# Optimization experiments

Hardware: AMD Instinct MI355X
Metric: run time of the kernel (lower is better)

Reference implementation:

```python
import math
import jax, jax.numpy as jnp
import numpy as np

K, B, T = 6, 8, 12
DIM = 256
DH = 64          # dim_head
NH = 8           # num_heads
G = 8            # offset_groups
INNER = DH * NH  # 512
HALF = INNER // 2  # 256
OFF_D = INNER // G  # 64
HBEV = WBEV = 256
PW = PH = 102.4   # x/y range extents
SCALE = DH ** -0.5
OFF_SCALE = 4.0


def setup_inputs() -> dict:
    key = jax.random.key(0)
    ks = jax.random.split(key, 20)
    w = lambda i, shape: jax.random.normal(ks[i], shape, jnp.float32) * 0.05
    return {
        "dec_embed": jax.random.normal(ks[0], (K, B, T, DIM), jnp.float32),
        "bev_feat": jax.random.normal(ks[1], (B, DIM, HBEV, WBEV), jnp.float32),
        "query_scale": jax.random.uniform(ks[2], (K, B, T, HALF), jnp.float32),
        "ref_points": (jax.random.uniform(ks[3], (K, B, T, 2), jnp.float32) * 2.0 - 1.0) * 51.2,
        "Wq": w(4, (DIM, HALF)), "bq": jnp.zeros((HALF,), jnp.float32),
        "Wk": w(5, (DIM, HALF)),
        "Wv": w(6, (DIM, HALF)),
        "pq_W1": w(7, (HALF, HALF)), "pq_b1": jnp.zeros((HALF,), jnp.float32),
        "pq_W2": w(8, (HALF, HALF)), "pq_b2": jnp.zeros((HALF,), jnp.float32),
        "pk_W1": w(9, (HALF, HALF)), "pk_b1": jnp.zeros((HALF,), jnp.float32),
        "pk_W2": w(10, (HALF, HALF)), "pk_b2": jnp.zeros((HALF,), jnp.float32),
        "off_W1": w(11, (OFF_D // 2, OFF_D)), "off_b1": jnp.zeros((OFF_D,), jnp.float32),
        "off_W2": w(12, (OFF_D, 2)), "off_b2": jnp.zeros((2,), jnp.float32),
        "out_W": w(13, (HALF, DIM)), "out_b": jnp.zeros((DIM,), jnp.float32),
    }


def _grid_sample(im, grid):
    """F.grid_sample, bilinear, padding_mode='zeros', align_corners=False.
    im: (B,C,H,W), grid: (B,Hg,Wg,2) with (x,y) in [-1,1]. Returns (B,C,Hg,Wg)."""
    Bn, C, Hh, Ww = im.shape
    gx, gy = grid[..., 0], grid[..., 1]
    ix = ((gx + 1.0) * Ww - 1.0) * 0.5
    iy = ((gy + 1.0) * Hh - 1.0) * 0.5
    ix0 = jnp.floor(ix)
    iy0 = jnp.floor(iy)
    wx = (ix - ix0)[:, None]  # (B,1,Hg,Wg)
    wy = (iy - iy0)[:, None]
    imf = im.reshape(Bn, C, Hh * Ww)

    def gather(xq, yq):
        valid = (xq >= 0) & (xq < Ww) & (yq >= 0) & (yq < Hh)
        idx = (jnp.clip(yq, 0, Hh - 1) * Ww + jnp.clip(xq, 0, Ww - 1)).astype(jnp.int32)
        v = jnp.take_along_axis(imf, idx.reshape(Bn, 1, -1), axis=2)
        v = v.reshape(Bn, C, *xq.shape[1:])
        return v * valid[:, None].astype(im.dtype)

    v00 = gather(ix0, iy0)
    v01 = gather(ix0 + 1, iy0)
    v10 = gather(ix0, iy0 + 1)
    v11 = gather(ix0 + 1, iy0 + 1)
    return (v00 * (1 - wx) * (1 - wy) + v01 * wx * (1 - wy)
            + v10 * (1 - wx) * wy + v11 * wx * wy)


def _sine_embed(pos, hidden=256, temp=40.0):
    """DAB-DETR style sine embedding for 2D positions. pos: (...,2) -> (...,hidden)."""
    half = hidden // 2
    dim_t = jnp.arange(half, dtype=pos.dtype)
    dim_t = temp ** (2.0 * jnp.floor(dim_t / 2.0) / half)
    sc = 2.0 * math.pi
    ex = pos[..., 0, None] * sc / dim_t
    ey = pos[..., 1, None] * sc / dim_t

    def interleave(e):
        return jnp.stack((jnp.sin(e[..., 0::2]), jnp.cos(e[..., 1::2])), axis=-1).reshape(*e.shape[:-1], -1)

    return jnp.concatenate((interleave(ey), interleave(ex)), axis=-1)


def reference(dec_embed, bev_feat, query_scale, ref_points,
              Wq, bq, Wk, Wv,
              pq_W1, pq_b1, pq_W2, pq_b2,
              pk_W1, pk_b1, pk_W2, pk_b2,
              off_W1, off_b1, off_W2, off_b2,
              out_W, out_b):
    de = dec_embed.transpose(1, 0, 2, 3)     # (B,K,T,D)
    qs = query_scale.transpose(1, 0, 2, 3)   # (B,K,T,256)
    rp = ref_points.transpose(1, 0, 2, 3)    # (B,K,T,2)
    Bn, Kn, Tn = de.shape[:3]

    con_q = de @ Wq + bq                                    # (B,K,T,256)
    oin = con_q.reshape(Bn, Kn, Tn, G, OFF_D // 2)          # (B,K,T,G,32)
    off = jax.nn.gelu(oin @ off_W1 + off_b1, approximate=False)
    off = jnp.tanh(off @ off_W2 + off_b2) * OFF_SCALE       # (B,K,T,G,2)

    vgrid = rp[..., None, :] + off                          # (B,K,T,G,2)
    vgrid = vgrid.reshape(Bn, Kn * Tn, G, 2)
    norm = jnp.array([2.0 / PW, 2.0 / PH], vgrid.dtype)
    vgrid_scaled = vgrid * norm                             # ref_from_Q normalization

    con_k_map = jnp.einsum('bchw,cd->bdhw', bev_feat, Wk)   # 1x1 conv, no bias
    v_map = jnp.einsum('bchw,cd->bdhw', bev_feat, Wv)
    con_k = _grid_sample(con_k_map, vgrid_scaled)           # (B,256,KT,G)
    v = _grid_sample(v_map, vgrid_scaled)                   # (B,256,KT,G)

    ref_scaled = rp * norm                                  # (B,K,T,2)
    qse = _sine_embed(ref_scaled)                           # (B,K,T,256)
    pos_q = (jax.nn.relu(qse @ pq_W1 + pq_b1) @ pq_W2 + pq_b2) * qs
    kse = _sine_embed(vgrid_scaled)                         # (B,KT,G,256)
    pos_k = jax.nn.relu(kse @ pk_W1 + pk_b1) @ pk_W2 + pk_b2

    BS = Bn * Kn * Tn
    dh = HALF // NH  # 32 per-head content dim
    cq = con_q.reshape(BS, 1, NH, dh)
    pq = pos_q.reshape(BS, 1, NH, dh)
    ck = con_k.transpose(0, 2, 3, 1).reshape(BS, G, NH, dh)
    pk = pos_k.reshape(BS, G, NH, dh)
    vv = v.transpose(0, 2, 3, 1).reshape(BS, G, NH, dh)

    q = jnp.concatenate([cq, pq], -1).transpose(0, 2, 1, 3) * SCALE  # (BS,NH,1,64)
    k = jnp.concatenate([ck, pk], -1).transpose(0, 2, 1, 3)          # (BS,NH,G,64)
    vv = vv.transpose(0, 2, 1, 3)                                    # (BS,NH,G,32)

    sim = jnp.einsum('bhid,bhjd->bhij', q, k)               # (BS,NH,1,G)
    attn = jax.nn.softmax(sim, axis=-1)
    out = jnp.einsum('bhij,bhjd->bhid', attn, vv)           # (BS,NH,1,32)

    out = out.transpose(0, 2, 1, 3).reshape(Bn, Kn, Tn, HALF).transpose(1, 0, 2, 3)
    out = out @ out_W + out_b                               # (K,B,T,D)
    return dec_embed + out
```

## Files before the change

kernel.cpp:

```cpp
#include <hip/hip_runtime.h>
#include <math.h>

#define NK 6
#define NB 8
#define NT 12
#define D 256
#define NG 8
#define NHD 8
#define HW 256
#define NQ (NK*NB*NT)

__global__ __launch_bounds__(256)
void dca_kernel(const float* __restrict__ dec_embed,
                const float* __restrict__ bev_feat,
                const float* __restrict__ query_scale,
                const float* __restrict__ ref_points,
                const float* __restrict__ Wq,     const float* __restrict__ bq,
                const float* __restrict__ Wk,     const float* __restrict__ Wv,
                const float* __restrict__ pq_W1,  const float* __restrict__ pq_b1,
                const float* __restrict__ pq_W2,  const float* __restrict__ pq_b2,
                const float* __restrict__ pk_W1,  const float* __restrict__ pk_b1,
                const float* __restrict__ pk_W2,  const float* __restrict__ pk_b2,
                const float* __restrict__ off_W1, const float* __restrict__ off_b1,
                const float* __restrict__ off_W2, const float* __restrict__ off_b2,
                const float* __restrict__ out_W,  const float* __restrict__ out_b,
                float* __restrict__ out)
{
    __shared__ float de[D];
    __shared__ float conq[D];
    __shared__ float qse[D];
    __shared__ float tmp1[D];
    __shared__ float posq[D];
    __shared__ float oatt[D];
    __shared__ float h1[NG][64];
    __shared__ float gxy[NG][2];
    __shared__ float sim[NHD][NG];
    __shared__ float bufA[NG][D];
    __shared__ float bufB[NG][D];
    __shared__ float conk[NG][D];
    __shared__ float vmat[NG][D];

    const int tid = threadIdx.x;
    const int q   = blockIdx.x;
    const int bb  = (q / NT) % NB;

    const float NORM = 0.01953125f;
    const float TWO_PI = 6.28318530717958647692f;
    const float L2_40_OVER_64 = 5.32192809488736234787f / 64.0f;

    de[tid] = dec_embed[(size_t)q * D + tid];
    __syncthreads();

    {
        float acc = bq[tid];
        #pragma unroll 4
        for (int i = 0; i < D; i += 4) {
            float4 d4 = *(const float4*)&de[i];
            acc += d4.x * Wq[(i + 0) * D + tid];
            acc += d4.y * Wq[(i + 1) * D + tid];
            acc += d4.z * Wq[(i + 2) * D + tid];
            acc += d4.w * Wq[(i + 3) * D + tid];
        }
        conq[tid] = acc;
    }
    __syncthreads();

    for (int idx = tid; idx < NG * 64; idx += 256) {
        int g = idx >> 6, j = idx & 63;
        float acc = off_b1[j];
        #pragma unroll
        for (int i = 0; i < 32; i += 4) {
            float4 c4 = *(const float4*)&conq[g * 32 + i];
            acc += c4.x * off_W1[(i + 0) * 64 + j];
            acc += c4.y * off_W1[(i + 1) * 64 + j];
            acc += c4.z * off_W1[(i + 2) * 64 + j];
            acc += c4.w * off_W1[(i + 3) * 64 + j];
        }
        h1[g][j] = 0.5f * acc * (1.0f + erff(acc * 0.70710678118654752440f));
    }
    __syncthreads();

    if (tid < NG * 2) {
        int g = tid >> 1, c = tid & 1;
        float acc = off_b2[c];
        #pragma unroll
        for (int j = 0; j < 64; j += 4) {
            float4 hh = *(const float4*)&h1[g][j];
            acc += hh.x * off_W2[(j + 0) * 2 + c];
            acc += hh.y * off_W2[(j + 1) * 2 + c];
            acc += hh.z * off_W2[(j + 2) * 2 + c];
            acc += hh.w * off_W2[(j + 3) * 2 + c];
        }
        float off = tanhf(acc) * 4.0f;
        float rp  = ref_points[(size_t)q * 2 + c];
        gxy[g][c] = (rp + off) * NORM;
    }
    __syncthreads();

    {
        const float* ch = bev_feat + ((size_t)bb * D + tid) * HW * HW;
        #pragma unroll
        for (int g = 0; g < NG; ++g) {
            float gx = gxy[g][0], gy = gxy[g][1];
            float ix = ((gx + 1.0f) * HW - 1.0f) * 0.5f;
            float iy = ((gy + 1.0f) * HW - 1.0f) * 0.5f;
            float fx0 = floorf(ix), fy0 = floorf(iy);
            float wx = ix - fx0, wy = iy - fy0;
            int x0 = (int)fx0, y0 = (int)fy0;
            bool xin0 = (x0 >= 0) && (x0 < HW);
            bool xin1 = (x0 + 1 >= 0) && (x0 + 1 < HW);
            bool yin0 = (y0 >= 0) && (y0 < HW);
            bool yin1 = (y0 + 1 >= 0) && (y0 + 1 < HW);
            float v00 = 0.f, v01 = 0.f, v10 = 0.f, v11 = 0.f;
            if (yin0) {
                if (xin0) v00 = ch[y0 * HW + x0];
                if (xin1) v01 = ch[y0 * HW + x0 + 1];
            }
            if (yin1) {
                if (xin0) v10 = ch[(y0 + 1) * HW + x0];
                if (xin1) v11 = ch[(y0 + 1) * HW + x0 + 1];
            }
            bufA[g][tid] = v00 * (1.f - wx) * (1.f - wy) + v01 * wx * (1.f - wy)
                         + v10 * (1.f - wx) * wy        + v11 * wx * wy;
        }
        {
            float rx = ref_points[(size_t)q * 2 + 0] * NORM;
            float ry = ref_points[(size_t)q * 2 + 1] * NORM;
            int j = tid;
            float pos = (j < 128) ? ry : rx;
            int m = (j & 127) >> 1;
            float freq = TWO_PI / exp2f((float)m * L2_40_OVER_64);
            float e = pos * freq;
            qse[j] = (j & 1) ? cosf(e) : sinf(e);
        }
        {
            int m = (tid & 127) >> 1;
            float freq = TWO_PI / exp2f((float)m * L2_40_OVER_64);
            #pragma unroll
            for (int g = 0; g < NG; ++g) {
                float pos = (tid < 128) ? gxy[g][1] : gxy[g][0];
                float e = pos * freq;
                bufB[g][tid] = (tid & 1) ? cosf(e) : sinf(e);
            }
        }
    }
    __syncthreads();

    {
        float accK[NG], accV[NG];
        #pragma unroll
        for (int g = 0; g < NG; ++g) { accK[g] = 0.f; accV[g] = 0.f; }
        #pragma unroll 2
        for (int i = 0; i < D; i += 4) {
            float wk0 = Wk[(i + 0) * D + tid], wk1 = Wk[(i + 1) * D + tid];
            float wk2 = Wk[(i + 2) * D + tid], wk3 = Wk[(i + 3) * D + tid];
            float wv0 = Wv[(i + 0) * D + tid], wv1 = Wv[(i + 1) * D + tid];
            float wv2 = Wv[(i + 2) * D + tid], wv3 = Wv[(i + 3) * D + tid];
            #pragma unroll
            for (int g = 0; g < NG; ++g) {
                float4 s = *(const float4*)&bufA[g][i];
                accK[g] += s.x * wk0 + s.y * wk1 + s.z * wk2 + s.w * wk3;
                accV[g] += s.x * wv0 + s.y * wv1 + s.z * wv2 + s.w * wv3;
            }
        }
        #pragma unroll
        for (int g = 0; g < NG; ++g) { conk[g][tid] = accK[g]; vmat[g][tid] = accV[g]; }
    }
    __syncthreads();

    {
        float acc[NG + 1];
        float biask = pk_b1[tid];
        #pragma unroll
        for (int g = 0; g < NG; ++g) acc[g] = biask;
        acc[NG] = pq_b1[tid];
        #pragma unroll 2
        for (int i = 0; i < D; i += 4) {
            float k0 = pk_W1[(i + 0) * D + tid], k1 = pk_W1[(i + 1) * D + tid];
            float k2 = pk_W1[(i + 2) * D + tid], k3 = pk_W1[(i + 3) * D + tid];
            float q0 = pq_W1[(i + 0) * D + tid], q1 = pq_W1[(i + 1) * D + tid];
            float q2 = pq_W1[(i + 2) * D + tid], q3 = pq_W1[(i + 3) * D + tid];
            #pragma unroll
            for (int g = 0; g < NG; ++g) {
                float4 s = *(const float4*)&bufB[g][i];
                acc[g] += s.x * k0 + s.y * k1 + s.z * k2 + s.w * k3;
            }
            float4 t = *(const float4*)&qse[i];
            acc[NG] += t.x * q0 + t.y * q1 + t.z * q2 + t.w * q3;
        }
        #pragma unroll
        for (int g = 0; g < NG; ++g) bufA[g][tid] = fmaxf(acc[g], 0.f);
        tmp1[tid] = fmaxf(acc[NG], 0.f);
    }
    __syncthreads();

    {
        float acc[NG + 1];
        float biask = pk_b2[tid];
        #pragma unroll
        for (int g = 0; g < NG; ++g) acc[g] = biask;
        acc[NG] = pq_b2[tid];
        #pragma unroll 2
        for (int i = 0; i < D; i += 4) {
            float k0 = pk_W2[(i + 0) * D + tid], k1 = pk_W2[(i + 1) * D + tid];
            float k2 = pk_W2[(i + 2) * D + tid], k3 = pk_W2[(i + 3) * D + tid];
            float q0 = pq_W2[(i + 0) * D + tid], q1 = pq_W2[(i + 1) * D + tid];
            float q2 = pq_W2[(i + 2) * D + tid], q3 = pq_W2[(i + 3) * D + tid];
            #pragma unroll
            for (int g = 0; g < NG; ++g) {
                float4 s = *(const float4*)&bufA[g][i];
                acc[g] += s.x * k0 + s.y * k1 + s.z * k2 + s.w * k3;
            }
            float4 t = *(const float4*)&tmp1[i];
            acc[NG] += t.x * q0 + t.y * q1 + t.z * q2 + t.w * q3;
        }
        #pragma unroll
        for (int g = 0; g < NG; ++g) bufB[g][tid] = acc[g];
        posq[tid] = acc[NG] * query_scale[(size_t)q * D + tid];
    }
    __syncthreads();

    if (tid < NHD * NG) {
        int h = tid >> 3, g = tid & 7;
        float s = 0.f;
        #pragma unroll
        for (int d = 0; d < 32; d += 4) {
            float4 a = *(const float4*)&conq[h * 32 + d];
            float4 b = *(const float4*)&conk[g][h * 32 + d];
            float4 c = *(const float4*)&posq[h * 32 + d];
            float4 e = *(const float4*)&bufB[g][h * 32 + d];
            s += a.x * b.x + a.y * b.y + a.z * b.z + a.w * b.w;
            s += c.x * e.x + c.y * e.y + c.z * e.z + c.w * e.w;
        }
        sim[h][g] = s * 0.125f;
    }
    __syncthreads();

    if (tid < NHD) {
        int h = tid;
        float mx = sim[h][0];
        for (int g = 1; g < NG; ++g) mx = fmaxf(mx, sim[h][g]);
        float ex[NG], sum = 0.f;
        #pragma unroll
        for (int g = 0; g < NG; ++g) { ex[g] = expf(sim[h][g] - mx); sum += ex[g]; }
        float inv = 1.0f / sum;
        #pragma unroll
        for (int g = 0; g < NG; ++g) sim[h][g] = ex[g] * inv;
    }
    __syncthreads();

    {
        int h = tid >> 5, d = tid & 31;
        float o = 0.f;
        #pragma unroll
        for (int g = 0; g < NG; ++g) o += sim[h][g] * vmat[g][h * 32 + d];
        oatt[tid] = o;
    }
    __syncthreads();

    {
        float acc = out_b[tid];
        #pragma unroll 4
        for (int i = 0; i < D; i += 4) {
            float4 o4 = *(const float4*)&oatt[i];
            acc += o4.x * out_W[(i + 0) * D + tid];
            acc += o4.y * out_W[(i + 1) * D + tid];
            acc += o4.z * out_W[(i + 2) * D + tid];
            acc += o4.w * out_W[(i + 3) * D + tid];
        }
        out[(size_t)q * D + tid] = acc + de[tid];
    }
}

extern "C" void kernel_launch(void* const* d_in, const int* in_sizes, int n_in,
                              void* d_out, int out_size, void* d_ws, size_t ws_size,
                              hipStream_t stream) {
    const float* dec_embed   = (const float*)d_in[0];
    const float* bev_feat    = (const float*)d_in[1];
    const float* query_scale = (const float*)d_in[2];
    const float* ref_points  = (const float*)d_in[3];
    const float* Wq     = (const float*)d_in[4];
    const float* bq     = (const float*)d_in[5];
    const float* Wk     = (const float*)d_in[6];
    const float* Wv     = (const float*)d_in[7];
    const float* pq_W1  = (const float*)d_in[8];
    const float* pq_b1  = (const float*)d_in[9];
    const float* pq_W2  = (const float*)d_in[10];
    const float* pq_b2  = (const float*)d_in[11];
    const float* pk_W1  = (const float*)d_in[12];
    const float* pk_b1  = (const float*)d_in[13];
    const float* pk_W2  = (const float*)d_in[14];
    const float* pk_b2  = (const float*)d_in[15];
    const float* off_W1 = (const float*)d_in[16];
    const float* off_b1 = (const float*)d_in[17];
    const float* off_W2 = (const float*)d_in[18];
    const float* off_b2 = (const float*)d_in[19];
    const float* out_W  = (const float*)d_in[20];
    const float* out_b  = (const float*)d_in[21];
    float* out = (float*)d_out;

    dca_kernel<<<NQ, 256, 0, stream>>>(dec_embed, bev_feat, query_scale, ref_points,
                                       Wq, bq, Wk, Wv,
                                       pq_W1, pq_b1, pq_W2, pq_b2,
                                       pk_W1, pk_b1, pk_W2, pk_b2,
                                       off_W1, off_b1, off_W2, off_b2,
                                       out_W, out_b, out);
}
```

Baseline: 737.2 us.

## Reassociate attention projections to skip per-group key/value and pos-key second-layer matmuls

The change reassociates the attention math. Each query is first projected through Wk (and pos_q through pk_W2) per head, so scores become dot products with the sampled features and with the hidden pos-key activations. This removes the per-group K/V projections and the pk_W2 second layer applied to all 8 groups. Values are handled by mixing the sampled features with the attention weights per head before one Wv matmul. The trade is extra transposed-row weight reads (strided float4 per thread), a partial-sum reduction step, padded shared arrays, and changed floating-point summation order.

Measured after the change: 731.3 us. Within noise of the previous version (-0.8%).

```diff
diff --git a/kernel.cpp b/kernel.cpp
--- a/kernel.cpp
+++ b/kernel.cpp
@@ -5,6 +5,7 @@
 #define NB 8
 #define NT 12
 #define D 256
+#define DP (D+4)
 #define NG 8
 #define NHD 8
 #define HW 256
@@ -35,10 +36,12 @@
     __shared__ float h1[NG][64];
     __shared__ float gxy[NG][2];
     __shared__ float sim[NHD][NG];
-    __shared__ float bufA[NG][D];
-    __shared__ float bufB[NG][D];
-    __shared__ float conk[NG][D];
-    __shared__ float vmat[NG][D];
+    __shared__ float psum[64][4];
+    __shared__ float samp[NG][DP];
+    __shared__ float kseW[NG][DP];
+    __shared__ float tmpk[NG][DP];
+    __shared__ float wqk [NHD][DP];
+    __shared__ float wqpk[NHD][DP];
 
     const int tid = threadIdx.x;
     const int q   = blockIdx.x;
@@ -62,6 +65,13 @@
             acc += d4.w * Wq[(i + 3) * D + tid];
         }
         conq[tid] = acc;
+        float rx = ref_points[(size_t)q * 2 + 0] * NORM;
+        float ry = ref_points[(size_t)q * 2 + 1] * NORM;
+        float pos = (tid < 128) ? ry : rx;
+        int m = (tid & 127) >> 1;
+        float freq = TWO_PI / exp2f((float)m * L2_40_OVER_64);
+        float e = pos * freq;
+        qse[tid] = (tid & 1) ? cosf(e) : sinf(e);
     }
     __syncthreads();
 
@@ -120,18 +130,8 @@
                 if (xin0) v10 = ch[(y0 + 1) * HW + x0];
                 if (xin1) v11 = ch[(y0 + 1) * HW + x0 + 1];
             }
-            bufA[g][tid] = v00 * (1.f - wx) * (1.f - wy) + v01 * wx * (1.f - wy)
+            samp[g][tid] = v00 * (1.f - wx) * (1.f - wy) + v01 * wx * (1.f - wy)
                          + v10 * (1.f - wx) * wy        + v11 * wx * wy;
-        }
-        {
-            float rx = ref_points[(size_t)q * 2 + 0] * NORM;
-            float ry = ref_points[(size_t)q * 2 + 1] * NORM;
-            int j = tid;
-            float pos = (j < 128) ? ry : rx;
-            int m = (j & 127) >> 1;
-            float freq = TWO_PI / exp2f((float)m * L2_40_OVER_64);
-            float e = pos * freq;
-            qse[j] = (j & 1) ? cosf(e) : sinf(e);
         }
         {
             int m = (tid & 127) >> 1;
@@ -140,31 +140,21 @@
             for (int g = 0; g < NG; ++g) {
                 float pos = (tid < 128) ? gxy[g][1] : gxy[g][0];
                 float e = pos * freq;
-                bufB[g][tid] = (tid & 1) ? cosf(e) : sinf(e);
-            }
-        }
-    }
-    __syncthreads();
-
-    {
-        float accK[NG], accV[NG];
-        #pragma unroll
-        for (int g = 0; g < NG; ++g) { accK[g] = 0.f; accV[g] = 0.f; }
-        #pragma unroll 2
-        for (int i = 0; i < D; i += 4) {
-            float wk0 = Wk[(i + 0) * D + tid], wk1 = Wk[(i + 1) * D + tid];
-            float wk2 = Wk[(i + 2) * D + tid], wk3 = Wk[(i + 3) * D + tid];
-            float wv0 = Wv[(i + 0) * D + tid], wv1 = Wv[(i + 1) * D + tid];
-            float wv2 = Wv[(i + 2) * D + tid], wv3 = Wv[(i + 3) * D + tid];
-            #pragma unroll
-            for (int g = 0; g < NG; ++g) {
-                float4 s = *(const float4*)&bufA[g][i];
-                accK[g] += s.x * wk0 + s.y * wk1 + s.z * wk2 + s.w * wk3;
-                accV[g] += s.x * wv0 + s.y * wv1 + s.z * wv2 + s.w * wv3;
-            }
-        }
-        #pragma unroll
-        for (int g = 0; g < NG; ++g) { conk[g][tid] = accK[g]; vmat[g][tid] = accV[g]; }
+                kseW[g][tid] = (tid & 1) ? cosf(e) : sinf(e);
+            }
+        }
+        {
+            float acc[NHD] = {0.f,0.f,0.f,0.f,0.f,0.f,0.f,0.f};
+            const float* wkrow = Wk + (size_t)tid * D;
+            #pragma unroll
+            for (int c = 0; c < D; c += 4) {
+                float4 w  = *(const float4*)&wkrow[c];
+                float4 cq = *(const float4*)&conq[c];
+                acc[c >> 5] += w.x * cq.x + w.y * cq.y + w.z * cq.z + w.w * cq.w;
+            }
+            #pragma unroll
+            for (int h = 0; h < NHD; ++h) wqk[h][tid] = acc[h];
+        }
     }
     __syncthreads();
 
@@ -182,57 +172,66 @@
             float q2 = pq_W1[(i + 2) * D + tid], q3 = pq_W1[(i + 3) * D + tid];
             #pragma unroll
             for (int g = 0; g < NG; ++g) {
-                float4 s = *(const float4*)&bufB[g][i];
+                float4 s = *(const float4*)&kseW[g][i];
                 acc[g] += s.x * k0 + s.y * k1 + s.z * k2 + s.w * k3;
             }
             float4 t = *(const float4*)&qse[i];
             acc[NG] += t.x * q0 + t.y * q1 + t.z * q2 + t.w * q3;
         }
         #pragma unroll
-        for (int g = 0; g < NG; ++g) bufA[g][tid] = fmaxf(acc[g], 0.f);
+        for (int g = 0; g < NG; ++g) tmpk[g][tid] = fmaxf(acc[g], 0.f);
         tmp1[tid] = fmaxf(acc[NG], 0.f);
     }
     __syncthreads();
 
     {
-        float acc[NG + 1];
-        float biask = pk_b2[tid];
-        #pragma unroll
-        for (int g = 0; g < NG; ++g) acc[g] = biask;
-        acc[NG] = pq_b2[tid];
-        #pragma unroll 2
-        for (int i = 0; i < D; i += 4) {
-            float k0 = pk_W2[(i + 0) * D + tid], k1 = pk_W2[(i + 1) * D + tid];
-            float k2 = pk_W2[(i + 2) * D + tid], k3 = pk_W2[(i + 3) * D + tid];
-            float q0 = pq_W2[(i + 0) * D + tid], q1 = pq_W2[(i + 1) * D + tid];
-            float q2 = pq_W2[(i + 2) * D + tid], q3 = pq_W2[(i + 3) * D + tid];
-            #pragma unroll
-            for (int g = 0; g < NG; ++g) {
-                float4 s = *(const float4*)&bufA[g][i];
-                acc[g] += s.x * k0 + s.y * k1 + s.z * k2 + s.w * k3;
-            }
+        float a2 = pq_b2[tid];
+        #pragma unroll 4
+        for (int i = 0; i < D; i += 4) {
             float4 t = *(const float4*)&tmp1[i];
-            acc[NG] += t.x * q0 + t.y * q1 + t.z * q2 + t.w * q3;
-        }
-        #pragma unroll
-        for (int g = 0; g < NG; ++g) bufB[g][tid] = acc[g];
-        posq[tid] = acc[NG] * query_scale[(size_t)q * D + tid];
-    }
-    __syncthreads();
-
-    if (tid < NHD * NG) {
-        int h = tid >> 3, g = tid & 7;
+            a2 += t.x * pq_W2[(i + 0) * D + tid];
+            a2 += t.y * pq_W2[(i + 1) * D + tid];
+            a2 += t.z * pq_W2[(i + 2) * D + tid];
+            a2 += t.w * pq_W2[(i + 3) * D + tid];
+        }
+        posq[tid] = a2 * query_scale[(size_t)q * D + tid];
+    }
+    __syncthreads();
+
+    {
+        float acc[NHD] = {0.f,0.f,0.f,0.f,0.f,0.f,0.f,0.f};
+        const float* wrow = pk_W2 + (size_t)tid * D;
+        #pragma unroll
+        for (int c = 0; c < D; c += 4) {
+            float4 w  = *(const float4*)&wrow[c];
+            float4 p4 = *(const float4*)&posq[c];
+            acc[c >> 5] += w.x * p4.x + w.y * p4.y + w.z * p4.z + w.w * p4.w;
+        }
+        #pragma unroll
+        for (int h = 0; h < NHD; ++h) wqpk[h][tid] = acc[h];
+    }
+    __syncthreads();
+
+    {
+        int pair = tid >> 2, part = tid & 3;
+        int h = pair >> 3, g = pair & 7;
+        int i0 = part * 64;
         float s = 0.f;
         #pragma unroll
-        for (int d = 0; d < 32; d += 4) {
-            float4 a = *(const float4*)&conq[h * 32 + d];
-            float4 b = *(const float4*)&conk[g][h * 32 + d];
-            float4 c = *(const float4*)&posq[h * 32 + d];
-            float4 e = *(const float4*)&bufB[g][h * 32 + d];
+        for (int i = i0; i < i0 + 64; i += 4) {
+            float4 a = *(const float4*)&samp[g][i];
+            float4 b = *(const float4*)&wqk[h][i];
+            float4 c = *(const float4*)&tmpk[g][i];
+            float4 d = *(const float4*)&wqpk[h][i];
             s += a.x * b.x + a.y * b.y + a.z * b.z + a.w * b.w;
-            s += c.x * e.x + c.y * e.y + c.z * e.z + c.w * e.w;
-        }
-        sim[h][g] = s * 0.125f;
+            s += c.x * d.x + c.y * d.y + c.z * d.z + c.w * d.w;
+        }
+        psum[pair][part] = s;
+    }
+    __syncthreads();
+    if (tid < 64) {
+        float s = psum[tid][0] + psum[tid][1] + psum[tid][2] + psum[tid][3];
+        sim[tid >> 3][tid & 7] = s * 0.125f;
     }
     __syncthreads();
 
@@ -250,11 +249,32 @@
     __syncthreads();
 
     {
-        int h = tid >> 5, d = tid & 31;
-        float o = 0.f;
-        #pragma unroll
-        for (int g = 0; g < NG; ++g) o += sim[h][g] * vmat[g][h * 32 + d];
-        oatt[tid] = o;
+        float ws[NHD];
+        #pragma unroll
+        for (int h = 0; h < NHD; ++h) ws[h] = 0.f;
+        #pragma unroll
+        for (int g = 0; g < NG; ++g) {
+            float sv = samp[g][tid];
+            #pragma unroll
+            for (int h = 0; h < NHD; ++h) ws[h] += sim[h][g] * sv;
+        }
+        #pragma unroll
+        for (int h = 0; h < NHD; ++h) kseW[h][tid] = ws[h];
+    }
+    __syncthreads();
+
+    {
+        int h = tid >> 5;
+        float acc = 0.f;
+        #pragma unroll 4
+        for (int i = 0; i < D; i += 4) {
+            float4 w4 = *(const float4*)&kseW[h][i];
+            acc += w4.x * Wv[(i + 0) * D + tid];
+            acc += w4.y * Wv[(i + 1) * D + tid];
+            acc += w4.z * Wv[(i + 2) * D + tid];
+            acc += w4.w * Wv[(i + 3) * D + tid];
+        }
+        oatt[tid] = acc;
     }
     __syncthreads();
 
```
